# Performance work log

Measured on AMD Instinct MI355X. Metric: run time of the kernel, lower is better.

Reference implementation:

```python
import jax, jax.numpy as jnp
import numpy as np

N, T, H, L, E, F, CN, CG = 20000, 2, 128, 4, 320000, 514, 3, 2
EPS = 1e-7  # GENConv message epsilon


def _ln(x, g, b):
    mu = jnp.mean(x, axis=-1, keepdims=True)
    var = jnp.mean((x - mu) ** 2, axis=-1, keepdims=True)
    return (x - mu) / jnp.sqrt(var + 1e-5) * g + b


def _genconv(x, src, dst, e, W1, b1, g1, be1, W2, b2, t, n):
    # message: relu(x_j + edge_attr) + eps
    msg = jax.nn.relu(x[src] + e) + EPS  # [E,H]
    # softmax aggregation with learnable temperature t, grouped by dst
    logits = msg * t
    m = jax.ops.segment_max(logits, dst, num_segments=n)
    m = jnp.where(jnp.isfinite(m), m, 0.0)  # guard empty segments
    ex = jnp.exp(logits - m[dst])
    denom = jax.ops.segment_sum(ex, dst, num_segments=n)
    alpha = ex / (denom[dst] + 1e-16)
    agg = jax.ops.segment_sum(msg * alpha, dst, num_segments=n)  # [N,H]
    out = agg + x  # residual with root node (x_r)
    # MLP: Lin(H,2H) -> LayerNorm -> ReLU -> Lin(2H,H)
    h1 = jax.nn.relu(_ln(out @ W1 + b1, g1, be1))
    return h1 @ W2 + b2


def _attn(x, Wq, Wk, Wv, gamma):
    # x: [N, T, H]; channel (transform-axis) self-attention, gamma-gated residual
    q = jnp.einsum('tc,nch->nth', Wq, x)
    k = jnp.einsum('tc,nch->nth', Wk, x)
    v = jnp.einsum('tc,nch->nth', Wv, x)
    a = jax.nn.softmax(jnp.einsum('nth,nsh->nts', q, k), axis=-1)
    o = jnp.einsum('nts,nsh->nth', a, v)
    return gamma * o + x


def setup_inputs() -> dict:
    key = jax.random.key(0)
    ks = iter(jax.random.split(key, 48))

    def nrm(sh, s=0.02):
        return jax.random.normal(next(ks), sh, dtype=jnp.float32) * s

    inp = {}
    inp['node_feature'] = jax.random.normal(next(ks), (N, F), dtype=jnp.float32)
    inp['edge_index'] = jax.random.randint(next(ks), (T, 2, E), 0, N, dtype=jnp.int32)
    inp['edge_attr'] = jax.random.normal(next(ks), (T, E, 2), dtype=jnp.float32)
    # encoders
    inp['Wne'] = nrm((F, H)); inp['bne'] = jnp.zeros((H,), jnp.float32)
    inp['Wee'] = nrm((2, H)); inp['bee'] = jnp.zeros((H,), jnp.float32)
    # per-layer GENConv MLP params (stacked over L)
    inp['W1'] = nrm((L, H, 2 * H)); inp['b1'] = jnp.zeros((L, 2 * H), jnp.float32)
    inp['g1'] = jnp.ones((L, 2 * H), jnp.float32); inp['be1'] = jnp.zeros((L, 2 * H), jnp.float32)
    inp['W2'] = nrm((L, 2 * H, H)); inp['b2'] = jnp.zeros((L, H), jnp.float32)
    # DeepGCNLayer LayerNorms
    inp['dg'] = jnp.ones((L, H), jnp.float32); inp['db'] = jnp.zeros((L, H), jnp.float32)
    # learnable temperatures
    inp['t'] = jnp.ones((L,), jnp.float32)
    # node attention + head
    inp['Wq_n'] = nrm((T, T), 0.2); inp['Wk_n'] = nrm((T, T), 0.2); inp['Wv_n'] = nrm((T, T), 0.2)
    inp['gamma_n'] = jnp.float32(0.5)
    inp['Wn1'] = nrm((T * H, T * H)); inp['bn1'] = jnp.zeros((T * H,), jnp.float32)
    inp['Wn2'] = nrm((T * H, CN)); inp['bn2'] = jnp.zeros((CN,), jnp.float32)
    # graph attention + head
    inp['Wq_g'] = nrm((T, T), 0.2); inp['Wk_g'] = nrm((T, T), 0.2); inp['Wv_g'] = nrm((T, T), 0.2)
    inp['gamma_g'] = jnp.float32(0.5)
    inp['Wg1'] = nrm((T * H, T * H)); inp['bg1'] = jnp.zeros((T * H,), jnp.float32)
    inp['Wg2'] = nrm((T * H, CG)); inp['bg2'] = jnp.zeros((CG,), jnp.float32)
    return inp


def reference(node_feature, edge_index, edge_attr, Wne, bne, Wee, bee,
              W1, b1, g1, be1, W2, b2, dg, db, t,
              Wq_n, Wk_n, Wv_n, gamma_n, Wn1, bn1, Wn2, bn2,
              Wq_g, Wk_g, Wv_g, gamma_g, Wg1, bg1, Wg2, bg2):
    embs = []
    for ti in range(T):
        x = node_feature @ Wne + bne           # node_encoder
        e = edge_attr[ti] @ Wee + bee          # edge_encoder
        src, dst = edge_index[ti, 0], edge_index[ti, 1]
        # layers[0].conv applied directly
        x = _genconv(x, src, dst, e, W1[0], b1[0], g1[0], be1[0], W2[0], b2[0], t[0], N)
        # res+ DeepGCN blocks
        for l in range(1, L):
            h = jax.nn.relu(_ln(x, dg[l], db[l]))  # dropout p=0.1 is identity in eval
            x = x + _genconv(h, src, dst, e, W1[l], b1[l], g1[l], be1[l], W2[l], b2[l], t[l], N)
        x = jax.nn.relu(_ln(x, dg[0], db[0]))
        embs.append(x)
    emb = jnp.stack(embs, axis=1)  # [N, T, H]

    a = _attn(emb, Wq_n, Wk_n, Wv_n, gamma_n).reshape(N, T * H)
    node = jax.nn.relu(a @ Wn1 + bn1) @ Wn2 + bn2
    node = jax.nn.log_softmax(node, axis=-1)

    g = _attn(emb, Wq_g, Wk_g, Wv_g, gamma_g).reshape(N, T * H)
    gp = jnp.mean(g, axis=0, keepdims=True)  # global_mean_pool (single graph)
    gp = jax.nn.relu(gp @ Wg1 + bg1) @ Wg2 + bg2
    gp = jax.nn.log_softmax(gp, axis=-1)
    return (node, gp)
```

## Files before the change

kernel.cpp:

```cpp
#include <hip/hip_runtime.h>

#define NN 20000
#define TT 2
#define HH 128
#define LL 4
#define EE 320000
#define FF 514
#define CN 3
#define CG 2
#define EPS_MSG 1e-7f
#define MP 20096

typedef __bf16 bf16x8 __attribute__((ext_vector_type(8)));
typedef __bf16 bf16x2 __attribute__((ext_vector_type(2)));
typedef float f32x4 __attribute__((ext_vector_type(4)));

struct __align__(8) Edge { int src; __bf16 ea0, ea1; };

__device__ inline float wave_sum(float v) {
#pragma unroll
  for (int off = 32; off; off >>= 1) v += __shfl_xor(v, off);
  return v;
}
__device__ inline float red16(float v) {
  v += __shfl_xor(v, 1); v += __shfl_xor(v, 2);
  v += __shfl_xor(v, 4); v += __shfl_xor(v, 8);
  return v;
}

__device__ __forceinline__ void gload_lds16(const void* g, void* l) {
  __builtin_amdgcn_global_load_lds(
      (const __attribute__((address_space(1))) unsigned int*)g,
      (__attribute__((address_space(3))) unsigned int*)l, 16, 0, 0);
}

template <typename OT>
__global__ __launch_bounds__(256) void gemm_mfma(
    const __bf16* __restrict__ A, const __bf16* __restrict__ BT,
    const float* __restrict__ bias, OT* __restrict__ C, int M, int N, int K,
    int dupRows) {
  __shared__ __bf16 As[2][64][32];
  __shared__ __bf16 Bs[2][128][32];
  const int tid = threadIdx.x;
  const int lane = tid & 63, w = tid >> 6;
  const int bm = blockIdx.y * 64, bn = blockIdx.x * 128;
  const int wr = (w >> 1) * 32, wc = (w & 1) * 64;
  const int fr = lane & 15, fq = lane >> 4;
  const int rowA = tid >> 2, chA = (tid & 3) * 8;
  const __bf16* Ab = A + (size_t)(bm + rowA) * K + chA;
  const __bf16* Bb = BT + (size_t)(bn + rowA) * K + chA;
  const __bf16* Bb2 = Bb + (size_t)64 * K;
  f32x4 acc[2][4] = {};

#define STAGE(buf, k0)                                  \
  do {                                                  \
    gload_lds16(Ab + (k0), &As[buf][rowA][chA]);        \
    gload_lds16(Bb + (k0), &Bs[buf][rowA][chA]);        \
    gload_lds16(Bb2 + (k0), &Bs[buf][rowA + 64][chA]);  \
  } while (0)

  STAGE(0, 0);
  __syncthreads();
  int cur = 0;
  for (int k0 = 0; k0 < K; k0 += 32) {
    if (k0 + 32 < K) STAGE(cur ^ 1, k0 + 32);
    bf16x8 af[2], bq[4];
#pragma unroll
    for (int m = 0; m < 2; ++m)
      af[m] = *(const bf16x8*)&As[cur][wr + m * 16 + fr][fq * 8];
#pragma unroll
    for (int n = 0; n < 4; ++n)
      bq[n] = *(const bf16x8*)&Bs[cur][wc + n * 16 + fr][fq * 8];
#pragma unroll
    for (int m = 0; m < 2; ++m)
#pragma unroll
      for (int n = 0; n < 4; ++n)
        acc[m][n] =
            __builtin_amdgcn_mfma_f32_16x16x32_bf16(af[m], bq[n], acc[m][n], 0, 0, 0);
    __syncthreads();
    cur ^= 1;
  }
#undef STAGE

#pragma unroll
  for (int m = 0; m < 2; ++m) {
#pragma unroll
    for (int n = 0; n < 4; ++n) {
#pragma unroll
      for (int j = 0; j < 4; ++j) {
        int gm = bm + wr + m * 16 + fq * 4 + j;
        int gn = bn + wc + n * 16 + fr;
        if (gm < M) {
          float c = acc[m][n][j] + bias[gn];
          C[(size_t)gm * N + gn] = (OT)c;
          if (dupRows) C[(size_t)(gm + dupRows) * N + gn] = (OT)c;
        }
      }
    }
  }
}

template <int EPI>
__global__ __launch_bounds__(256) void gemm256(
    const __bf16* __restrict__ A, const __bf16* __restrict__ BT,
    const float* __restrict__ bias, const float* __restrict__ g,
    const float* __restrict__ be, const float* __restrict__ W2h,
    const float* __restrict__ b2h, void* __restrict__ outp, int M, int K) {
  __shared__ __bf16 As[2][64][32];
  __shared__ __bf16 Bs[2][256][32];
  const int tid = threadIdx.x;
  const int lane = tid & 63, w = tid >> 6;
  const int bm = blockIdx.x * 64;
  const int wr = w * 16;
  const int fr = lane & 15, fq = lane >> 4;
  const int rowA = tid >> 2, chA = (tid & 3) * 8;
  const __bf16* Ab = A + (size_t)(bm + rowA) * K + chA;
  const __bf16* Bb = BT + (size_t)rowA * K + chA;
  f32x4 acc[16] = {};

#define STG(buf, k0)                                                \
  do {                                                              \
    gload_lds16(Ab + (k0), &As[buf][rowA][chA]);                    \
    _Pragma("unroll") for (int r = 0; r < 4; ++r)                   \
        gload_lds16(Bb + (size_t)(r * 64) * K + (k0),               \
                    &Bs[buf][rowA + r * 64][chA]);                  \
  } while (0)

  STG(0, 0);
  __syncthreads();
  int cur = 0;
  for (int k0 = 0; k0 < K; k0 += 32) {
    if (k0 + 32 < K) STG(cur ^ 1, k0 + 32);
    bf16x8 af = *(const bf16x8*)&As[cur][wr + fr][fq * 8];
#pragma unroll
    for (int n = 0; n < 16; ++n) {
      bf16x8 bq = *(const bf16x8*)&Bs[cur][n * 16 + fr][fq * 8];
      acc[n] = __builtin_amdgcn_mfma_f32_16x16x32_bf16(af, bq, acc[n], 0, 0, 0);
    }
    __syncthreads();
    cur ^= 1;
  }
#undef STG

  float cb[16];
#pragma unroll
  for (int n = 0; n < 16; ++n) cb[n] = bias[n * 16 + fr];

  if constexpr (EPI == 0) {
    float gv[16], bev[16];
#pragma unroll
    for (int n = 0; n < 16; ++n) {
      gv[n] = g[n * 16 + fr];
      bev[n] = be[n * 16 + fr];
    }
    __bf16* outb = (__bf16*)outp;
#pragma unroll
    for (int j = 0; j < 4; ++j) {
      float cj[16], s = 0.f, s2 = 0.f;
#pragma unroll
      for (int n = 0; n < 16; ++n) {
        float c = acc[n][j] + cb[n];
        cj[n] = c; s += c; s2 += c * c;
      }
      s = red16(s); s2 = red16(s2);
      float mu = s * (1.f / 256);
      float var = fmaxf(s2 * (1.f / 256) - mu * mu, 0.f);
      float rr = rsqrtf(var + 1e-5f);
      int gm = bm + wr + fq * 4 + j;
      __bf16* op = outb + (size_t)gm * 256;
#pragma unroll
      for (int n = 0; n < 16; ++n) {
        float y = (cj[n] - mu) * rr * gv[n] + bev[n];
        op[n * 16 + fr] = (__bf16)fmaxf(y, 0.f);
      }
    }
  } else {
    float w0[16], w1[16], w2[16];
#pragma unroll
    for (int n = 0; n < 16; ++n) {
      int col = n * 16 + fr;
      w0[n] = W2h[col * 3 + 0];
      w1[n] = W2h[col * 3 + 1];
      w2[n] = W2h[col * 3 + 2];
    }
    float* outf = (float*)outp;
#pragma unroll
    for (int j = 0; j < 4; ++j) {
      float p0 = 0.f, p1 = 0.f, p2 = 0.f;
#pragma unroll
      for (int n = 0; n < 16; ++n) {
        float h = fmaxf(acc[n][j] + cb[n], 0.f);
        p0 += h * w0[n]; p1 += h * w1[n]; p2 += h * w2[n];
      }
      p0 = red16(p0); p1 = red16(p1); p2 = red16(p2);
      int gm = bm + wr + fq * 4 + j;
      if (fr == 0 && gm < M) {
        float l0 = p0 + b2h[0], l1 = p1 + b2h[1], l2 = p2 + b2h[2];
        float m = fmaxf(l0, fmaxf(l1, l2));
        float lse = m + logf(__expf(l0 - m) + __expf(l1 - m) + __expf(l2 - m));
        outf[(size_t)gm * 3 + 0] = l0 - lse;
        outf[(size_t)gm * 3 + 1] = l1 - lse;
        outf[(size_t)gm * 3 + 2] = l2 - lse;
      }
    }
  }
}

template <int MODE>
__global__ __launch_bounds__(256) void gemm_lin2(
    const __bf16* __restrict__ A, const __bf16* __restrict__ BT,
    const float* __restrict__ bias, float* __restrict__ xres,
    const float* __restrict__ g, const float* __restrict__ be,
    void* __restrict__ lnout) {
  __shared__ __bf16 As[2][64][32];
  __shared__ __bf16 Bs[2][128][32];
  __shared__ float redS[64][2], redS2[64][2];
  const int tid = threadIdx.x;
  const int lane = tid & 63, w = tid >> 6;
  const int bm = blockIdx.x * 64;
  const int wr = (w >> 1) * 32, wc = (w & 1) * 64;
  const int fr = lane & 15, fq = lane >> 4;
  const int rowA = tid >> 2, chA = (tid & 3) * 8;
  const __bf16* Ab = A + (size_t)(bm + rowA) * 256 + chA;
  const __bf16* Bb = BT + (size_t)rowA * 256 + chA;
  const __bf16* Bb2 = Bb + (size_t)64 * 256;
  f32x4 acc[2][4] = {};

#define STAGE(buf, k0)                                  \
  do {                                                  \
    gload_lds16(Ab + (k0), &As[buf][rowA][chA]);        \
    gload_lds16(Bb + (k0), &Bs[buf][rowA][chA]);        \
    gload_lds16(Bb2 + (k0), &Bs[buf][rowA + 64][chA]);  \
  } while (0)

  STAGE(0, 0);
  __syncthreads();
  int cur = 0;
  for (int k0 = 0; k0 < 256; k0 += 32) {
    if (k0 + 32 < 256) STAGE(cur ^ 1, k0 + 32);
    bf16x8 af[2], bq[4];
#pragma unroll
    for (int m = 0; m < 2; ++m)
      af[m] = *(const bf16x8*)&As[cur][wr + m * 16 + fr][fq * 8];
#pragma unroll
    for (int n = 0; n < 4; ++n)
      bq[n] = *(const bf16x8*)&Bs[cur][wc + n * 16 + fr][fq * 8];
#pragma unroll
    for (int m = 0; m < 2; ++m)
#pragma unroll
      for (int n = 0; n < 4; ++n)
        acc[m][n] =
            __builtin_amdgcn_mfma_f32_16x16x32_bf16(af[m], bq[n], acc[m][n], 0, 0, 0);
    __syncthreads();
    cur ^= 1;
  }
#undef STAGE

  float cv[2][4][4];
#pragma unroll
  for (int m = 0; m < 2; ++m) {
    int r0 = wr + m * 16 + fq * 4;
#pragma unroll
    for (int j = 0; j < 4; ++j) {
      int gm = bm + r0 + j;
      float s = 0.f, s2 = 0.f;
#pragma unroll
      for (int n = 0; n < 4; ++n) {
        float c = acc[m][n][j] + bias[wc + n * 16 + fr];
        if (MODE != 0) c += xres[(size_t)gm * 128 + wc + n * 16 + fr];
        cv[m][n][j] = c;
        s += c; s2 += c * c;
      }
      s = red16(s); s2 = red16(s2);
      if (fr == 0) {
        redS[r0 + j][w & 1] = s;
        redS2[r0 + j][w & 1] = s2;
      }
    }
  }
  __syncthreads();
#pragma unroll
  for (int m = 0; m < 2; ++m) {
    int r0 = wr + m * 16 + fq * 4;
#pragma unroll
    for (int j = 0; j < 4; ++j) {
      int r = r0 + j;
      int gm = bm + r;
      float S = redS[r][0] + redS[r][1];
      float S2 = redS2[r][0] + redS2[r][1];
      float mu = S * (1.f / 128);
      float var = fmaxf(S2 * (1.f / 128) - mu * mu, 0.f);
      float rr = rsqrtf(var + 1e-5f);
      if constexpr (MODE < 2) {
        float* xp = xres + (size_t)gm * 128;
        __bf16* hp = (__bf16*)lnout + (size_t)gm * 128;
#pragma unroll
        for (int n = 0; n < 4; ++n) {
          int col = wc + n * 16 + fr;
          float c = cv[m][n][j];
          xp[col] = c;
          float y = (c - mu) * rr * g[col] + be[col];
          hp[col] = (__bf16)fmaxf(y, 0.f);
        }
      } else {
        int half = gm >= MP;
        int node = gm - half * MP;
        if (node < NN) {
          float* ep = (float*)lnout + (size_t)node * 256 + half * 128;
#pragma unroll
          for (int n = 0; n < 4; ++n) {
            int col = wc + n * 16 + fr;
            float y = (cv[m][n][j] - mu) * rr * g[col] + be[col];
            ep[col] = fmaxf(y, 0.f);
          }
        }
      }
    }
  }
}

__global__ void nf_convert_kernel(const float* __restrict__ src, __bf16* __restrict__ dst) {
  int idx = blockIdx.x * 256 + threadIdx.x;
  if (idx >= NN * 576) return;
  int row = idx / 576, col = idx - row * 576;
  float v = (col < FF) ? src[(size_t)row * FF + col] : 0.f;
  dst[idx] = (__bf16)v;
}

struct WtDesc { const float* src; __bf16* dst; int K, N, Kpad; };
struct WtDescs { WtDesc d[10]; };

__global__ void wt_convert_kernel(WtDescs descs) {
  WtDesc de = descs.d[blockIdx.y];
  int idx = blockIdx.x * 256 + threadIdx.x;
  if (idx >= de.N * de.Kpad) return;
  int n = idx / de.Kpad, k = idx - n * de.Kpad;
  float v = (k < de.K) ? de.src[(size_t)k * de.N + n] : 0.f;
  de.dst[idx] = (__bf16)v;
}

__global__ void count2_kernel(const int* __restrict__ edge_index, int* __restrict__ deg) {
  int i = blockIdx.x * 256 + threadIdx.x;
  if (i >= 2 * EE) return;
  int ti = (i >= EE) ? 1 : 0;
  int e = i - ti * EE;
  int d = edge_index[(size_t)ti * 2 * EE + EE + e];
  atomicAdd(&deg[ti * NN + d], 1);
}

__global__ __launch_bounds__(1024) void scan2_kernel(
    const int* __restrict__ deg_all, int* __restrict__ rowptr,
    int* __restrict__ cursor) {
  const int ti = blockIdx.x;
  const int* deg = deg_all + ti * NN;
  __shared__ int sums[1024];
  int tid = threadIdx.x;
  int chunk = (NN + 1023) / 1024;
  int begin = tid * chunk, end = min(begin + chunk, NN);
  int s = 0;
  for (int i = begin; i < end; ++i) s += deg[i];
  sums[tid] = s;
  __syncthreads();
  for (int off = 1; off < 1024; off <<= 1) {
    int v = (tid >= off) ? sums[tid - off] : 0;
    __syncthreads();
    sums[tid] += v;
    __syncthreads();
  }
  int running = ti * EE + sums[tid] - s;
  for (int i = begin; i < end; ++i) {
    rowptr[ti * NN + i] = running;
    cursor[ti * NN + i] = running;
    running += deg[i];
  }
  if (tid == 0 && ti == 1) rowptr[2 * NN] = 2 * EE;
}

__global__ void scatter2_kernel(const int* __restrict__ edge_index,
                                const float* __restrict__ edge_attr,
                                int* __restrict__ cursor,
                                Edge* __restrict__ edges) {
  int i = blockIdx.x * 256 + threadIdx.x;
  if (i >= 2 * EE) return;
  int ti = (i >= EE) ? 1 : 0;
  int e = i - ti * EE;
  const int* srcp = edge_index + (size_t)ti * 2 * EE;
  int s = srcp[e], d = srcp[EE + e];
  float2 ea = ((const float2*)edge_attr)[(size_t)ti * EE + e];
  int pos = atomicAdd(&cursor[ti * NN + d], 1);
  Edge ed;
  ed.src = s + ti * MP;
  ed.ea0 = (__bf16)ea.x; ed.ea1 = (__bf16)ea.y;
  __builtin_memcpy(&edges[pos], &ed, sizeof(Edge));
}

__global__ __launch_bounds__(256) void agg_kernel(
    const __bf16* __restrict__ xin, const int* __restrict__ rowptr,
    const Edge* __restrict__ edges, const float* __restrict__ Wee,
    const float* __restrict__ bee, const float* __restrict__ tptr, int layer,
    __bf16* __restrict__ out) {
  int wave = threadIdx.x >> 6, lane = threadIdx.x & 63;
  int gnode = blockIdx.x * 4 + wave;
  if (gnode >= 2 * NN) return;
  int half = gnode >= NN;
  int xrow = half ? (gnode - NN + MP) : gnode;
  float t = tptr[layer];
  int c0 = lane * 2;
  float w00 = Wee[c0], w01 = Wee[c0 + 1];
  float w10 = Wee[HH + c0], w11 = Wee[HH + c0 + 1];
  float be0 = bee[c0], be1 = bee[c0 + 1];
  float denA0 = 0.f, denA1 = 0.f, numA0 = 0.f, numA1 = 0.f;
  float denB0 = 0.f, denB1 = 0.f, numB0 = 0.f, numB1 = 0.f;
  int e = rowptr[gnode], e1 = rowptr[gnode + 1];

#define MLP(XV, ED, D0, D1, N0, N1)                                      \
  do {                                                                   \
    float eax = (float)(ED).ea0, eay = (float)(ED).ea1;                  \
    float m0 = (float)(XV)[0] + eax * w00 + eay * w10 + be0;             \
    float m1 = (float)(XV)[1] + eax * w01 + eay * w11 + be1;             \
    m0 = fmaxf(m0, 0.f) + EPS_MSG;                                       \
    m1 = fmaxf(m1, 0.f) + EPS_MSG;                                       \
    float ex0 = __expf(m0 * t), ex1 = __expf(m1 * t);                    \
    D0 += ex0; D1 += ex1; N0 += m0 * ex0; N1 += m1 * ex1;                \
  } while (0)

  for (; e + 4 <= e1; e += 4) {
    Edge E0 = edges[e], E1 = edges[e + 1], E2 = edges[e + 2], E3 = edges[e + 3];
    bf16x2 x0 = *(const bf16x2*)(xin + (size_t)E0.src * HH + c0);
    bf16x2 x1 = *(const bf16x2*)(xin + (size_t)E1.src * HH + c0);
    bf16x2 x2 = *(const bf16x2*)(xin + (size_t)E2.src * HH + c0);
    bf16x2 x3 = *(const bf16x2*)(xin + (size_t)E3.src * HH + c0);
    MLP(x0, E0, denA0, denA1, numA0, numA1);
    MLP(x1, E1, denB0, denB1, numB0, numB1);
    MLP(x2, E2, denA0, denA1, numA0, numA1);
    MLP(x3, E3, denB0, denB1, numB0, numB1);
  }
  for (; e < e1; ++e) {
    Edge E0 = edges[e];
    bf16x2 x0 = *(const bf16x2*)(xin + (size_t)E0.src * HH + c0);
    MLP(x0, E0, denA0, denA1, numA0, numA1);
  }
#undef MLP
  float den0 = denA0 + denB0, den1 = denA1 + denB1;
  float num0 = numA0 + numB0, num1 = numA1 + numB1;
  bf16x2 xr = *(const bf16x2*)(xin + (size_t)xrow * HH + c0);
  bf16x2 o;
  o[0] = (__bf16)(num0 / (den0 + 1e-16f) + (float)xr[0]);
  o[1] = (__bf16)(num1 / (den1 + 1e-16f) + (float)xr[1]);
  *(bf16x2*)(out + (size_t)xrow * HH + c0) = o;
}

template <typename OT>
__global__ __launch_bounds__(256) void attn_kernel(
    const float* __restrict__ emb, const float* __restrict__ Wq,
    const float* __restrict__ Wk, const float* __restrict__ Wv,
    const float* __restrict__ gammap, OT* __restrict__ out, int nNodes) {
  int wave = threadIdx.x >> 6, lane = threadIdx.x & 63;
  int n = blockIdx.x * 4 + wave;
  if (n >= nNodes) return;
  float gamma = *gammap;
  float wq00 = Wq[0], wq01 = Wq[1], wq10 = Wq[2], wq11 = Wq[3];
  float wk00 = Wk[0], wk01 = Wk[1], wk10 = Wk[2], wk11 = Wk[3];
  float wv00 = Wv[0], wv01 = Wv[1], wv10 = Wv[2], wv11 = Wv[3];
  int c0 = lane * 2;
  const float* base = emb + (size_t)n * (2 * HH);
  float2 x0 = *(const float2*)(base + c0);
  float2 x1 = *(const float2*)(base + HH + c0);
  float q0a = wq00 * x0.x + wq01 * x1.x, q0b = wq00 * x0.y + wq01 * x1.y;
  float q1a = wq10 * x0.x + wq11 * x1.x, q1b = wq10 * x0.y + wq11 * x1.y;
  float k0a = wk00 * x0.x + wk01 * x1.x, k0b = wk00 * x0.y + wk01 * x1.y;
  float k1a = wk10 * x0.x + wk11 * x1.x, k1b = wk10 * x0.y + wk11 * x1.y;
  float v0a = wv00 * x0.x + wv01 * x1.x, v0b = wv00 * x0.y + wv01 * x1.y;
  float v1a = wv10 * x0.x + wv11 * x1.x, v1b = wv10 * x0.y + wv11 * x1.y;
  float s00 = wave_sum(q0a * k0a + q0b * k0b);
  float s01 = wave_sum(q0a * k1a + q0b * k1b);
  float s10 = wave_sum(q1a * k0a + q1b * k0b);
  float s11 = wave_sum(q1a * k1a + q1b * k1b);
  float m0 = fmaxf(s00, s01);
  float e00 = __expf(s00 - m0), e01 = __expf(s01 - m0);
  float i0 = 1.f / (e00 + e01);
  float a00 = e00 * i0, a01 = e01 * i0;
  float m1 = fmaxf(s10, s11);
  float e10 = __expf(s10 - m1), e11 = __expf(s11 - m1);
  float i1 = 1.f / (e10 + e11);
  float a10 = e10 * i1, a11 = e11 * i1;
  OT* op = out + (size_t)n * (2 * HH);
  op[c0] = (OT)(gamma * (a00 * v0a + a01 * v1a) + x0.x);
  op[c0 + 1] = (OT)(gamma * (a00 * v0b + a01 * v1b) + x0.y);
  op[HH + c0] = (OT)(gamma * (a10 * v0a + a11 * v1a) + x1.x);
  op[HH + c0 + 1] = (OT)(gamma * (a10 * v0b + a11 * v1b) + x1.y);
}

__global__ __launch_bounds__(256) void pool_kernel(const float* __restrict__ gbuf,
                                                   float* __restrict__ gp_sum, int nNodes) {
  int c = threadIdx.x;
  float s = 0.f;
  for (int r = blockIdx.x; r < nNodes; r += gridDim.x) s += gbuf[(size_t)r * 256 + c];
  atomicAdd(&gp_sum[c], s);
}

__global__ __launch_bounds__(256) void graph_head_kernel(
    const float* __restrict__ gp_sum, const float* __restrict__ Wg1,
    const float* __restrict__ bg1, const float* __restrict__ Wg2,
    const float* __restrict__ bg2, float* __restrict__ outp, float invN) {
  __shared__ float gp[256];
  __shared__ float h1[256];
  __shared__ float lg[2];
  int tid = threadIdx.x;
  gp[tid] = gp_sum[tid] * invN;
  __syncthreads();
  float acc = bg1[tid];
  for (int k = 0; k < 256; ++k) acc += gp[k] * Wg1[k * 256 + tid];
  h1[tid] = fmaxf(acc, 0.f);
  __syncthreads();
  if (tid < 2) {
    float l = bg2[tid];
    for (int c = 0; c < 256; ++c) l += h1[c] * Wg2[c * 2 + tid];
    lg[tid] = l;
  }
  __syncthreads();
  if (tid == 0) {
    float m = fmaxf(lg[0], lg[1]);
    float lse = m + logf(__expf(lg[0] - m) + __expf(lg[1] - m));
    outp[0] = lg[0] - lse;
    outp[1] = lg[1] - lse;
  }
}

extern "C" void kernel_launch(void* const* d_in, const int* in_sizes, int n_in,
                              void* d_out, int out_size, void* d_ws, size_t ws_size,
                              hipStream_t stream) {
  (void)in_sizes; (void)n_in; (void)out_size; (void)ws_size;
  const float* node_feature = (const float*)d_in[0];
  const int* edge_index = (const int*)d_in[1];
  const float* edge_attr = (const float*)d_in[2];
  const float* Wne = (const float*)d_in[3];
  const float* bne = (const float*)d_in[4];
  const float* Wee = (const float*)d_in[5];
  const float* bee = (const float*)d_in[6];
  const float* W1 = (const float*)d_in[7];
  const float* b1 = (const float*)d_in[8];
  const float* g1 = (const float*)d_in[9];
  const float* be1 = (const float*)d_in[10];
  const float* W2 = (const float*)d_in[11];
  const float* b2 = (const float*)d_in[12];
  const float* dg = (const float*)d_in[13];
  const float* db = (const float*)d_in[14];
  const float* tpar = (const float*)d_in[15];
  const float* Wq_n = (const float*)d_in[16];
  const float* Wk_n = (const float*)d_in[17];
  const float* Wv_n = (const float*)d_in[18];
  const float* gamma_n = (const float*)d_in[19];
  const float* Wn1 = (const float*)d_in[20];
  const float* bn1 = (const float*)d_in[21];
  const float* Wn2 = (const float*)d_in[22];
  const float* bn2 = (const float*)d_in[23];
  const float* Wq_g = (const float*)d_in[24];
  const float* Wk_g = (const float*)d_in[25];
  const float* Wv_g = (const float*)d_in[26];
  const float* gamma_g = (const float*)d_in[27];
  const float* Wg1 = (const float*)d_in[28];
  const float* bg1 = (const float*)d_in[29];
  const float* Wg2 = (const float*)d_in[30];
  const float* bg2 = (const float*)d_in[31];
  float* out = (float*)d_out;

  char* pc = (char*)d_ws;
  auto alloc = [&](size_t bytes) {
    char* r = pc;
    pc += (bytes + 255) & ~(size_t)255;
    return r;
  };
  float* xbuf = (float*)alloc((size_t)2 * MP * HH * 4);
  __bf16* hbuf_b = (__bf16*)alloc((size_t)2 * MP * HH * 2);
  __bf16* t256_b = (__bf16*)alloc((size_t)2 * MP * 256 * 2);
  float* emb = (float*)alloc((size_t)NN * 2 * HH * 4);
  __bf16* aggout_b = (__bf16*)alloc((size_t)2 * MP * HH * 2);
  __bf16* nf_b = (__bf16*)emb;
  __bf16* attnb = t256_b;
  float* buf2 = xbuf;
  __bf16* wt_ne = (__bf16*)alloc((size_t)128 * 576 * 2);
  __bf16* wt1 = (__bf16*)alloc((size_t)4 * 256 * 128 * 2);
  __bf16* wt2 = (__bf16*)alloc((size_t)4 * 128 * 256 * 2);
  __bf16* wtn1 = (__bf16*)alloc((size_t)256 * 256 * 2);
  float* gp_sum = (float*)alloc(256 * 4);
  int* deg = (int*)alloc((size_t)2 * NN * 4);
  int* cursor = (int*)alloc((size_t)2 * NN * 4);
  int* rowptr = (int*)alloc((size_t)(2 * NN + 2) * 4);
  Edge* edges = (Edge*)alloc((size_t)2 * EE * 8);

  const int rows4n = (NN + 3) / 4;
  const int rows4x = (2 * NN + 3) / 4;
  const int gRows2 = 2 * MP / 64;

  nf_convert_kernel<<<(NN * 576 + 255) / 256, 256, 0, stream>>>(node_feature, nf_b);
  WtDescs wd;
  wd.d[0] = {Wne, wt_ne, FF, HH, 576};
  for (int l = 0; l < 4; ++l)
    wd.d[1 + l] = {W1 + (size_t)l * HH * 256, wt1 + (size_t)l * 256 * HH, HH, 256, HH};
  for (int l = 0; l < 4; ++l)
    wd.d[5 + l] = {W2 + (size_t)l * 256 * HH, wt2 + (size_t)l * HH * 256, 256, HH, 256};
  wd.d[9] = {Wn1, wtn1, 256, 256, 256};
  wt_convert_kernel<<<dim3((128 * 576 + 255) / 256, 10), 256, 0, stream>>>(wd);

  hipMemsetAsync(deg, 0, 2 * NN * sizeof(int), stream);
  count2_kernel<<<(2 * EE + 255) / 256, 256, 0, stream>>>(edge_index, deg);
  scan2_kernel<<<2, 1024, 0, stream>>>(deg, rowptr, cursor);
  scatter2_kernel<<<(2 * EE + 255) / 256, 256, 0, stream>>>(edge_index, edge_attr,
                                                            cursor, edges);

  gemm_mfma<__bf16><<<dim3(1, MP / 64), 256, 0, stream>>>(nf_b, wt_ne, bne, hbuf_b,
                                                          NN, HH, 576, MP);

  for (int l = 0; l < LL; ++l) {
    agg_kernel<<<rows4x, 256, 0, stream>>>(hbuf_b, rowptr, edges, Wee, bee, tpar, l,
                                           aggout_b);
    gemm256<0><<<gRows2, 256, 0, stream>>>(aggout_b, wt1 + (size_t)l * 256 * HH,
                                           b1 + l * 2 * HH, g1 + l * 2 * HH,
                                           be1 + l * 2 * HH, nullptr, nullptr, t256_b,
                                           2 * MP, HH);
    const __bf16* w2l = wt2 + (size_t)l * HH * 256;
    const float* b2l = b2 + l * HH;
    if (l == 0)
      gemm_lin2<0><<<gRows2, 256, 0, stream>>>(t256_b, w2l, b2l, xbuf, dg + 1 * HH,
                                               db + 1 * HH, hbuf_b);
    else if (l < LL - 1)
      gemm_lin2<1><<<gRows2, 256, 0, stream>>>(t256_b, w2l, b2l, xbuf,
                                               dg + (l + 1) * HH, db + (l + 1) * HH,
                                               hbuf_b);
    else
      gemm_lin2<2><<<gRows2, 256, 0, stream>>>(t256_b, w2l, b2l, xbuf, dg, db, emb);
  }

  attn_kernel<__bf16><<<rows4n, 256, 0, stream>>>(emb, Wq_n, Wk_n, Wv_n, gamma_n,
                                                  attnb, NN);
  gemm256<1><<<MP / 64, 256, 0, stream>>>(attnb, wtn1, bn1, nullptr, nullptr, Wn2,
                                          bn2, out, NN, 256);

  attn_kernel<float><<<rows4n, 256, 0, stream>>>(emb, Wq_g, Wk_g, Wv_g, gamma_g, buf2,
                                                 NN);
  hipMemsetAsync(gp_sum, 0, 256 * sizeof(float), stream);
  pool_kernel<<<128, 256, 0, stream>>>(buf2, gp_sum, NN);
  graph_head_kernel<<<1, 256, 0, stream>>>(gp_sum, Wg1, bg1, Wg2, bg2,
                                           out + (size_t)NN * CN, 1.0f / NN);
}
```

Measured before the change: 512.9 us.

## Fuse prep and setup kernels, merge attention passes, and rework aggregation lane mapping

Node-feature conversion, weight transposes, degree counting and the gp_sum clear are merged into one prep kernel. The edge scatter is folded into the encoder GEMM launch as extra blocks, and the two attention kernels become one pass that reads emb once. The aggregation kernel now has each lane handle 4 channels over two edges at a time with a cross-half shuffle reduction, and it remaps block indices to interleave the two graph halves. The intent is fewer launches and fewer memory passes, at the cost of more complex kernels and a mix of heterogeneous work inside single launches.

```diff
diff --git a/kernel.cpp b/kernel.cpp
--- a/kernel.cpp
+++ b/kernel.cpp
@@ -12,6 +12,7 @@
 #define MP 20096
 
 typedef __bf16 bf16x8 __attribute__((ext_vector_type(8)));
+typedef __bf16 bf16x4 __attribute__((ext_vector_type(4)));
 typedef __bf16 bf16x2 __attribute__((ext_vector_type(2)));
 typedef float f32x4 __attribute__((ext_vector_type(4)));
 
@@ -34,31 +35,46 @@
       (__attribute__((address_space(3))) unsigned int*)l, 16, 0, 0);
 }
 
-template <typename OT>
-__global__ __launch_bounds__(256) void gemm_mfma(
+#define ENCB (MP / 64)
+__global__ __launch_bounds__(256) void enc_scatter_kernel(
     const __bf16* __restrict__ A, const __bf16* __restrict__ BT,
-    const float* __restrict__ bias, OT* __restrict__ C, int M, int N, int K,
-    int dupRows) {
+    const float* __restrict__ bias, __bf16* __restrict__ C,
+    const int* __restrict__ edge_index, const float* __restrict__ edge_attr,
+    int* __restrict__ cursor, Edge* __restrict__ edges) {
   __shared__ __bf16 As[2][64][32];
   __shared__ __bf16 Bs[2][128][32];
   const int tid = threadIdx.x;
+  if (blockIdx.x >= ENCB) {
+    int i = (blockIdx.x - ENCB) * 256 + tid;
+    if (i >= 2 * EE) return;
+    int ti = (i >= EE) ? 1 : 0;
+    int e = i - ti * EE;
+    const int* srcp = edge_index + (size_t)ti * 2 * EE;
+    int s = srcp[e], d = srcp[EE + e];
+    float2 ea = ((const float2*)edge_attr)[(size_t)ti * EE + e];
+    int pos = atomicAdd(&cursor[ti * NN + d], 1);
+    Edge ed;
+    ed.src = s + ti * MP;
+    ed.ea0 = (__bf16)ea.x; ed.ea1 = (__bf16)ea.y;
+    __builtin_memcpy(&edges[pos], &ed, sizeof(Edge));
+    return;
+  }
+  const int K = 576;
   const int lane = tid & 63, w = tid >> 6;
-  const int bm = blockIdx.y * 64, bn = blockIdx.x * 128;
+  const int bm = blockIdx.x * 64;
   const int wr = (w >> 1) * 32, wc = (w & 1) * 64;
   const int fr = lane & 15, fq = lane >> 4;
   const int rowA = tid >> 2, chA = (tid & 3) * 8;
   const __bf16* Ab = A + (size_t)(bm + rowA) * K + chA;
-  const __bf16* Bb = BT + (size_t)(bn + rowA) * K + chA;
+  const __bf16* Bb = BT + (size_t)rowA * K + chA;
   const __bf16* Bb2 = Bb + (size_t)64 * K;
   f32x4 acc[2][4] = {};
-
 #define STAGE(buf, k0)                                  \
   do {                                                  \
     gload_lds16(Ab + (k0), &As[buf][rowA][chA]);        \
     gload_lds16(Bb + (k0), &Bs[buf][rowA][chA]);        \
     gload_lds16(Bb2 + (k0), &Bs[buf][rowA + 64][chA]);  \
   } while (0)
-
   STAGE(0, 0);
   __syncthreads();
   int cur = 0;
@@ -81,7 +97,6 @@
     cur ^= 1;
   }
 #undef STAGE
-
 #pragma unroll
   for (int m = 0; m < 2; ++m) {
 #pragma unroll
@@ -89,11 +104,11 @@
 #pragma unroll
       for (int j = 0; j < 4; ++j) {
         int gm = bm + wr + m * 16 + fq * 4 + j;
-        int gn = bn + wc + n * 16 + fr;
-        if (gm < M) {
-          float c = acc[m][n][j] + bias[gn];
-          C[(size_t)gm * N + gn] = (OT)c;
-          if (dupRows) C[(size_t)(gm + dupRows) * N + gn] = (OT)c;
+        int gn = wc + n * 16 + fr;
+        if (gm < NN) {
+          __bf16 c = (__bf16)(acc[m][n][j] + bias[gn]);
+          C[(size_t)gm * 128 + gn] = c;
+          C[(size_t)(gm + MP) * 128 + gn] = c;
         }
       }
     }
@@ -319,33 +334,40 @@
   }
 }
 
-__global__ void nf_convert_kernel(const float* __restrict__ src, __bf16* __restrict__ dst) {
-  int idx = blockIdx.x * 256 + threadIdx.x;
-  if (idx >= NN * 576) return;
-  int row = idx / 576, col = idx - row * 576;
-  float v = (col < FF) ? src[(size_t)row * FF + col] : 0.f;
-  dst[idx] = (__bf16)v;
-}
-
 struct WtDesc { const float* src; __bf16* dst; int K, N, Kpad; };
 struct WtDescs { WtDesc d[10]; };
-
-__global__ void wt_convert_kernel(WtDescs descs) {
-  WtDesc de = descs.d[blockIdx.y];
-  int idx = blockIdx.x * 256 + threadIdx.x;
-  if (idx >= de.N * de.Kpad) return;
-  int n = idx / de.Kpad, k = idx - n * de.Kpad;
-  float v = (k < de.K) ? de.src[(size_t)k * de.N + n] : 0.f;
-  de.dst[idx] = (__bf16)v;
-}
-
-__global__ void count2_kernel(const int* __restrict__ edge_index, int* __restrict__ deg) {
-  int i = blockIdx.x * 256 + threadIdx.x;
-  if (i >= 2 * EE) return;
-  int ti = (i >= EE) ? 1 : 0;
-  int e = i - ti * EE;
-  int d = edge_index[(size_t)ti * 2 * EE + EE + e];
-  atomicAdd(&deg[ti * NN + d], 1);
+#define NFB 45000
+#define WTB 2880
+#define CNTB 2500
+
+__global__ void prep_kernel(const float* __restrict__ nf_src,
+                            __bf16* __restrict__ nf_dst, WtDescs descs,
+                            const int* __restrict__ edge_index,
+                            int* __restrict__ deg, float* __restrict__ gp_sum) {
+  int b = blockIdx.x, tid = threadIdx.x;
+  if (b < NFB) {
+    int idx = b * 256 + tid;
+    int row = idx / 576, col = idx - row * 576;
+    float v = (col < FF) ? nf_src[(size_t)row * FF + col] : 0.f;
+    nf_dst[idx] = (__bf16)v;
+  } else if (b < NFB + WTB) {
+    int wb = b - NFB;
+    WtDesc de = descs.d[wb / 288];
+    int idx = (wb % 288) * 256 + tid;
+    if (idx >= de.N * de.Kpad) return;
+    int n = idx / de.Kpad, k = idx - n * de.Kpad;
+    float v = (k < de.K) ? de.src[(size_t)k * de.N + n] : 0.f;
+    de.dst[idx] = (__bf16)v;
+  } else if (b < NFB + WTB + CNTB) {
+    int i = (b - NFB - WTB) * 256 + tid;
+    if (i >= 2 * EE) return;
+    int ti = (i >= EE) ? 1 : 0;
+    int e = i - ti * EE;
+    int d = edge_index[(size_t)ti * 2 * EE + EE + e];
+    atomicAdd(&deg[ti * NN + d], 1);
+  } else {
+    gp_sum[tid] = 0.f;
+  }
 }
 
 __global__ __launch_bounds__(1024) void scan2_kernel(
@@ -376,119 +398,136 @@
   if (tid == 0 && ti == 1) rowptr[2 * NN] = 2 * EE;
 }
 
-__global__ void scatter2_kernel(const int* __restrict__ edge_index,
-                                const float* __restrict__ edge_attr,
-                                int* __restrict__ cursor,
-                                Edge* __restrict__ edges) {
-  int i = blockIdx.x * 256 + threadIdx.x;
-  if (i >= 2 * EE) return;
-  int ti = (i >= EE) ? 1 : 0;
-  int e = i - ti * EE;
-  const int* srcp = edge_index + (size_t)ti * 2 * EE;
-  int s = srcp[e], d = srcp[EE + e];
-  float2 ea = ((const float2*)edge_attr)[(size_t)ti * EE + e];
-  int pos = atomicAdd(&cursor[ti * NN + d], 1);
-  Edge ed;
-  ed.src = s + ti * MP;
-  ed.ea0 = (__bf16)ea.x; ed.ea1 = (__bf16)ea.y;
-  __builtin_memcpy(&edges[pos], &ed, sizeof(Edge));
-}
-
 __global__ __launch_bounds__(256) void agg_kernel(
     const __bf16* __restrict__ xin, const int* __restrict__ rowptr,
     const Edge* __restrict__ edges, const float* __restrict__ Wee,
     const float* __restrict__ bee, const float* __restrict__ tptr, int layer,
     __bf16* __restrict__ out) {
   int wave = threadIdx.x >> 6, lane = threadIdx.x & 63;
-  int gnode = blockIdx.x * 4 + wave;
-  if (gnode >= 2 * NN) return;
-  int half = gnode >= NN;
-  int xrow = half ? (gnode - NN + MP) : gnode;
+  int b = blockIdx.x;
+  int h8 = b & 7;
+  int half = h8 >> 2;
+  int within = (b >> 3) * 4 + (h8 & 3);
+  int node = within * 4 + wave;
+  int gnode = half * NN + node;
+  int xrow = half * MP + node;
   float t = tptr[layer];
-  int c0 = lane * 2;
-  float w00 = Wee[c0], w01 = Wee[c0 + 1];
-  float w10 = Wee[HH + c0], w11 = Wee[HH + c0 + 1];
-  float be0 = bee[c0], be1 = bee[c0 + 1];
-  float denA0 = 0.f, denA1 = 0.f, numA0 = 0.f, numA1 = 0.f;
-  float denB0 = 0.f, denB1 = 0.f, numB0 = 0.f, numB1 = 0.f;
+  int hh = lane >> 5, c32 = lane & 31, c0 = c32 * 4;
+  float w0[4], w1[4], bv[4];
+#pragma unroll
+  for (int i = 0; i < 4; ++i) {
+    w0[i] = Wee[c0 + i];
+    w1[i] = Wee[HH + c0 + i];
+    bv[i] = bee[c0 + i];
+  }
+  float den[4] = {}, num[4] = {};
   int e = rowptr[gnode], e1 = rowptr[gnode + 1];
 
-#define MLP(XV, ED, D0, D1, N0, N1)                                      \
-  do {                                                                   \
-    float eax = (float)(ED).ea0, eay = (float)(ED).ea1;                  \
-    float m0 = (float)(XV)[0] + eax * w00 + eay * w10 + be0;             \
-    float m1 = (float)(XV)[1] + eax * w01 + eay * w11 + be1;             \
-    m0 = fmaxf(m0, 0.f) + EPS_MSG;                                       \
-    m1 = fmaxf(m1, 0.f) + EPS_MSG;                                       \
-    float ex0 = __expf(m0 * t), ex1 = __expf(m1 * t);                    \
-    D0 += ex0; D1 += ex1; N0 += m0 * ex0; N1 += m1 * ex1;                \
+#define MLP4(XV, ED)                                              \
+  do {                                                            \
+    float eax = (float)(ED).ea0, eay = (float)(ED).ea1;           \
+    _Pragma("unroll") for (int i = 0; i < 4; ++i) {               \
+      float m = (float)(XV)[i] + eax * w0[i] + eay * w1[i] + bv[i]; \
+      m = fmaxf(m, 0.f) + EPS_MSG;                                \
+      float ex = __expf(m * t);                                   \
+      den[i] += ex; num[i] += m * ex;                             \
+    }                                                             \
   } while (0)
 
   for (; e + 4 <= e1; e += 4) {
-    Edge E0 = edges[e], E1 = edges[e + 1], E2 = edges[e + 2], E3 = edges[e + 3];
-    bf16x2 x0 = *(const bf16x2*)(xin + (size_t)E0.src * HH + c0);
-    bf16x2 x1 = *(const bf16x2*)(xin + (size_t)E1.src * HH + c0);
-    bf16x2 x2 = *(const bf16x2*)(xin + (size_t)E2.src * HH + c0);
-    bf16x2 x3 = *(const bf16x2*)(xin + (size_t)E3.src * HH + c0);
-    MLP(x0, E0, denA0, denA1, numA0, numA1);
-    MLP(x1, E1, denB0, denB1, numB0, numB1);
-    MLP(x2, E2, denA0, denA1, numA0, numA1);
-    MLP(x3, E3, denB0, denB1, numB0, numB1);
-  }
-  for (; e < e1; ++e) {
-    Edge E0 = edges[e];
-    bf16x2 x0 = *(const bf16x2*)(xin + (size_t)E0.src * HH + c0);
-    MLP(x0, E0, denA0, denA1, numA0, numA1);
-  }
-#undef MLP
-  float den0 = denA0 + denB0, den1 = denA1 + denB1;
-  float num0 = numA0 + numB0, num1 = numA1 + numB1;
-  bf16x2 xr = *(const bf16x2*)(xin + (size_t)xrow * HH + c0);
-  bf16x2 o;
-  o[0] = (__bf16)(num0 / (den0 + 1e-16f) + (float)xr[0]);
-  o[1] = (__bf16)(num1 / (den1 + 1e-16f) + (float)xr[1]);
-  *(bf16x2*)(out + (size_t)xrow * HH + c0) = o;
-}
-
-template <typename OT>
-__global__ __launch_bounds__(256) void attn_kernel(
-    const float* __restrict__ emb, const float* __restrict__ Wq,
-    const float* __restrict__ Wk, const float* __restrict__ Wv,
-    const float* __restrict__ gammap, OT* __restrict__ out, int nNodes) {
+    Edge Ea = edges[e + hh];
+    Edge Eb = edges[e + 2 + hh];
+    bf16x4 xa = *(const bf16x4*)(xin + (size_t)Ea.src * HH + c0);
+    bf16x4 xb = *(const bf16x4*)(xin + (size_t)Eb.src * HH + c0);
+    MLP4(xa, Ea);
+    MLP4(xb, Eb);
+  }
+  if (e + hh < e1) {
+    Edge Ea = edges[e + hh];
+    bf16x4 xa = *(const bf16x4*)(xin + (size_t)Ea.src * HH + c0);
+    MLP4(xa, Ea);
+  }
+  if (e + 2 + hh < e1) {
+    Edge Ea = edges[e + 2 + hh];
+    bf16x4 xa = *(const bf16x4*)(xin + (size_t)Ea.src * HH + c0);
+    MLP4(xa, Ea);
+  }
+#undef MLP4
+
+#pragma unroll
+  for (int i = 0; i < 4; ++i) {
+    den[i] += __shfl_xor(den[i], 32);
+    num[i] += __shfl_xor(num[i], 32);
+  }
+  if (hh == 0) {
+    bf16x4 xr = *(const bf16x4*)(xin + (size_t)xrow * HH + c0);
+    bf16x4 o;
+#pragma unroll
+    for (int i = 0; i < 4; ++i)
+      o[i] = (__bf16)(num[i] / (den[i] + 1e-16f) + (float)xr[i]);
+    *(bf16x4*)(out + (size_t)xrow * HH + c0) = o;
+  }
+}
+
+__global__ __launch_bounds__(256) void attn2_kernel(
+    const float* __restrict__ emb, const float* __restrict__ Wq_n,
+    const float* __restrict__ Wk_n, const float* __restrict__ Wv_n,
+    const float* __restrict__ gn, const float* __restrict__ Wq_g,
+    const float* __restrict__ Wk_g, const float* __restrict__ Wv_g,
+    const float* __restrict__ gg, __bf16* __restrict__ outn,
+    float* __restrict__ outg, int nNodes) {
   int wave = threadIdx.x >> 6, lane = threadIdx.x & 63;
   int n = blockIdx.x * 4 + wave;
   if (n >= nNodes) return;
-  float gamma = *gammap;
-  float wq00 = Wq[0], wq01 = Wq[1], wq10 = Wq[2], wq11 = Wq[3];
-  float wk00 = Wk[0], wk01 = Wk[1], wk10 = Wk[2], wk11 = Wk[3];
-  float wv00 = Wv[0], wv01 = Wv[1], wv10 = Wv[2], wv11 = Wv[3];
   int c0 = lane * 2;
   const float* base = emb + (size_t)n * (2 * HH);
   float2 x0 = *(const float2*)(base + c0);
   float2 x1 = *(const float2*)(base + HH + c0);
-  float q0a = wq00 * x0.x + wq01 * x1.x, q0b = wq00 * x0.y + wq01 * x1.y;
-  float q1a = wq10 * x0.x + wq11 * x1.x, q1b = wq10 * x0.y + wq11 * x1.y;
-  float k0a = wk00 * x0.x + wk01 * x1.x, k0b = wk00 * x0.y + wk01 * x1.y;
-  float k1a = wk10 * x0.x + wk11 * x1.x, k1b = wk10 * x0.y + wk11 * x1.y;
-  float v0a = wv00 * x0.x + wv01 * x1.x, v0b = wv00 * x0.y + wv01 * x1.y;
-  float v1a = wv10 * x0.x + wv11 * x1.x, v1b = wv10 * x0.y + wv11 * x1.y;
-  float s00 = wave_sum(q0a * k0a + q0b * k0b);
-  float s01 = wave_sum(q0a * k1a + q0b * k1b);
-  float s10 = wave_sum(q1a * k0a + q1b * k0b);
-  float s11 = wave_sum(q1a * k1a + q1b * k1b);
-  float m0 = fmaxf(s00, s01);
-  float e00 = __expf(s00 - m0), e01 = __expf(s01 - m0);
-  float i0 = 1.f / (e00 + e01);
-  float a00 = e00 * i0, a01 = e01 * i0;
-  float m1 = fmaxf(s10, s11);
-  float e10 = __expf(s10 - m1), e11 = __expf(s11 - m1);
-  float i1 = 1.f / (e10 + e11);
-  float a10 = e10 * i1, a11 = e11 * i1;
-  OT* op = out + (size_t)n * (2 * HH);
-  op[c0] = (OT)(gamma * (a00 * v0a + a01 * v1a) + x0.x);
-  op[c0 + 1] = (OT)(gamma * (a00 * v0b + a01 * v1b) + x0.y);
-  op[HH + c0] = (OT)(gamma * (a10 * v0a + a11 * v1a) + x1.x);
-  op[HH + c0 + 1] = (OT)(gamma * (a10 * v0b + a11 * v1b) + x1.y);
+
+#define ATTN_BODY(Wq, Wk, Wv, GAM, O0A, O0B, O1A, O1B)                        \
+  {                                                                           \
+    float gamma = *(GAM);                                                     \
+    float wq00 = Wq[0], wq01 = Wq[1], wq10 = Wq[2], wq11 = Wq[3];             \
+    float wk00 = Wk[0], wk01 = Wk[1], wk10 = Wk[2], wk11 = Wk[3];             \
+    float wv00 = Wv[0], wv01 = Wv[1], wv10 = Wv[2], wv11 = Wv[3];             \
+    float q0a = wq00 * x0.x + wq01 * x1.x, q0b = wq00 * x0.y + wq01 * x1.y;   \
+    float q1a = wq10 * x0.x + wq11 * x1.x, q1b = wq10 * x0.y + wq11 * x1.y;   \
+    float k0a = wk00 * x0.x + wk01 * x1.x, k0b = wk00 * x0.y + wk01 * x1.y;   \
+    float k1a = wk10 * x0.x + wk11 * x1.x, k1b = wk10 * x0.y + wk11 * x1.y;   \
+    float v0a = wv00 * x0.x + wv01 * x1.x, v0b = wv00 * x0.y + wv01 * x1.y;   \
+    float v1a = wv10 * x0.x + wv11 * x1.x, v1b = wv10 * x0.y + wv11 * x1.y;   \
+    float s00 = wave_sum(q0a * k0a + q0b * k0b);                              \
+    float s01 = wave_sum(q0a * k1a + q0b * k1b);                              \
+    float s10 = wave_sum(q1a * k0a + q1b * k0b);                              \
+    float s11 = wave_sum(q1a * k1a + q1b * k1b);                              \
+    float m0 = fmaxf(s00, s01);                                               \
+    float e00 = __expf(s00 - m0), e01 = __expf(s01 - m0);                     \
+    float i0 = 1.f / (e00 + e01);                                             \
+    float a00 = e00 * i0, a01 = e01 * i0;                                     \
+    float m1 = fmaxf(s10, s11);                                               \
+    float e10 = __expf(s10 - m1), e11 = __expf(s11 - m1);                     \
+    float i1 = 1.f / (e10 + e11);                                             \
+    float a10 = e10 * i1, a11 = e11 * i1;                                     \
+    O0A = gamma * (a00 * v0a + a01 * v1a) + x0.x;                             \
+    O0B = gamma * (a00 * v0b + a01 * v1b) + x0.y;                             \
+    O1A = gamma * (a10 * v0a + a11 * v1a) + x1.x;                             \
+    O1B = gamma * (a10 * v0b + a11 * v1b) + x1.y;                             \
+  }
+
+  float n0a, n0b, n1a, n1b;
+  ATTN_BODY(Wq_n, Wk_n, Wv_n, gn, n0a, n0b, n1a, n1b);
+  __bf16* opn = outn + (size_t)n * (2 * HH);
+  bf16x2 t0; t0[0] = (__bf16)n0a; t0[1] = (__bf16)n0b;
+  bf16x2 t1; t1[0] = (__bf16)n1a; t1[1] = (__bf16)n1b;
+  *(bf16x2*)(opn + c0) = t0;
+  *(bf16x2*)(opn + HH + c0) = t1;
+
+  float g0a, g0b, g1a, g1b;
+  ATTN_BODY(Wq_g, Wk_g, Wv_g, gg, g0a, g0b, g1a, g1b);
+  float* opg = outg + (size_t)n * (2 * HH);
+  *(float2*)(opg + c0) = make_float2(g0a, g0b);
+  *(float2*)(opg + HH + c0) = make_float2(g1a, g1b);
+#undef ATTN_BODY
 }
 
 __global__ __launch_bounds__(256) void pool_kernel(const float* __restrict__ gbuf,
@@ -589,11 +628,8 @@
   int* rowptr = (int*)alloc((size_t)(2 * NN + 2) * 4);
   Edge* edges = (Edge*)alloc((size_t)2 * EE * 8);
 
-  const int rows4n = (NN + 3) / 4;
-  const int rows4x = (2 * NN + 3) / 4;
   const int gRows2 = 2 * MP / 64;
 
-  nf_convert_kernel<<<(NN * 576 + 255) / 256, 256, 0, stream>>>(node_feature, nf_b);
   WtDescs wd;
   wd.d[0] = {Wne, wt_ne, FF, HH, 576};
   for (int l = 0; l < 4; ++l)
@@ -601,20 +637,17 @@
   for (int l = 0; l < 4; ++l)
     wd.d[5 + l] = {W2 + (size_t)l * 256 * HH, wt2 + (size_t)l * HH * 256, 256, HH, 256};
   wd.d[9] = {Wn1, wtn1, 256, 256, 256};
-  wt_convert_kernel<<<dim3((128 * 576 + 255) / 256, 10), 256, 0, stream>>>(wd);
 
   hipMemsetAsync(deg, 0, 2 * NN * sizeof(int), stream);
-  count2_kernel<<<(2 * EE + 255) / 256, 256, 0, stream>>>(edge_index, deg);
+  prep_kernel<<<NFB + WTB + CNTB + 1, 256, 0, stream>>>(node_feature, nf_b, wd,
+                                                        edge_index, deg, gp_sum);
   scan2_kernel<<<2, 1024, 0, stream>>>(deg, rowptr, cursor);
-  scatter2_kernel<<<(2 * EE + 255) / 256, 256, 0, stream>>>(edge_index, edge_attr,
-                                                            cursor, edges);
-
-  gemm_mfma<__bf16><<<dim3(1, MP / 64), 256, 0, stream>>>(nf_b, wt_ne, bne, hbuf_b,
-                                                          NN, HH, 576, MP);
+  enc_scatter_kernel<<<ENCB + CNTB, 256, 0, stream>>>(
+      nf_b, wt_ne, bne, hbuf_b, edge_index, edge_attr, cursor, edges);
 
   for (int l = 0; l < LL; ++l) {
-    agg_kernel<<<rows4x, 256, 0, stream>>>(hbuf_b, rowptr, edges, Wee, bee, tpar, l,
-                                           aggout_b);
+    agg_kernel<<<2 * NN / 4, 256, 0, stream>>>(hbuf_b, rowptr, edges, Wee, bee, tpar,
+                                               l, aggout_b);
     gemm256<0><<<gRows2, 256, 0, stream>>>(aggout_b, wt1 + (size_t)l * 256 * HH,
                                            b1 + l * 2 * HH, g1 + l * 2 * HH,
                                            be1 + l * 2 * HH, nullptr, nullptr, t256_b,
@@ -632,14 +665,11 @@
       gemm_lin2<2><<<gRows2, 256, 0, stream>>>(t256_b, w2l, b2l, xbuf, dg, db, emb);
   }
 
-  attn_kernel<__bf16><<<rows4n, 256, 0, stream>>>(emb, Wq_n, Wk_n, Wv_n, gamma_n,
-                                                  attnb, NN);
+  attn2_kernel<<<(NN + 3) / 4, 256, 0, stream>>>(emb, Wq_n, Wk_n, Wv_n, gamma_n,
+                                                 Wq_g, Wk_g, Wv_g, gamma_g, attnb,
+                                                 buf2, NN);
   gemm256<1><<<MP / 64, 256, 0, stream>>>(attnb, wtn1, bn1, nullptr, nullptr, Wn2,
                                           bn2, out, NN, 256);
-
-  attn_kernel<float><<<rows4n, 256, 0, stream>>>(emb, Wq_g, Wk_g, Wv_g, gamma_g, buf2,
-                                                 NN);
-  hipMemsetAsync(gp_sum, 0, 256 * sizeof(float), stream);
   pool_kernel<<<128, 256, 0, stream>>>(buf2, gp_sum, NN);
   graph_head_kernel<<<1, 256, 0, stream>>>(gp_sum, Wg1, bg1, Wg2, bg2,
                                            out + (size_t)NN * CN, 1.0f / NN);
```

New measurement: 507.4 us. No clear change (-1.1%).
